# Kernel tuning notes

Measured on AMD Instinct MI355X. Metric: run time of the kernel, lower is better.

## Reference

```python
import jax, jax.numpy as jnp
import numpy as np
import math

D_MODEL = 1024
N_HEAD = 16
HEAD_DIM = D_MODEL // N_HEAD


def setup_inputs() -> dict:
    key = jax.random.key(0)
    ks = jax.random.split(key, 9)
    B, S = 2, 2048
    x = jax.random.normal(ks[0], (B, S, D_MODEL), dtype=jnp.float32)
    # nn.Linear weights are [out, in]; default-ish init scale 0.02, phase projs std=0.005
    w = lambda k, std: jax.random.normal(k, (D_MODEL, D_MODEL), dtype=jnp.float32) * std
    return {
        "x": x,
        "Wq_amp": w(ks[1], 0.02),
        "Wk_amp": w(ks[2], 0.02),
        "Wq_phi": w(ks[3], 0.005),
        "Wk_phi": w(ks[4], 0.005),
        "Wv": w(ks[5], 0.02),
        "Wo": w(ks[6], 0.02),
        "score_log_scale": jnp.zeros((N_HEAD,), dtype=jnp.float32),
    }


def _split_heads(t):
    B, S, _ = t.shape
    return t.reshape(B, S, N_HEAD, HEAD_DIM).transpose(0, 2, 1, 3)  # [B,H,S,hd]


def reference(x, Wq_amp, Wk_amp, Wq_phi, Wk_phi, Wv, Wo, score_log_scale):
    B, S, _ = x.shape
    eps = 1e-6
    # amplitude (softplus) and phase (pi * tanh) projections
    q_amp = _split_heads(jax.nn.softplus(x @ Wq_amp.T))
    k_amp = _split_heads(jax.nn.softplus(x @ Wk_amp.T))
    q_phi = _split_heads(math.pi * jnp.tanh(x @ Wq_phi.T))
    k_phi = _split_heads(math.pi * jnp.tanh(x @ Wk_phi.T))
    # RMS-normalize amplitudes over head_dim
    q_amp = q_amp / jnp.sqrt(jnp.mean(q_amp * q_amp, axis=-1, keepdims=True) + eps)
    k_amp = k_amp / jnp.sqrt(jnp.mean(k_amp * k_amp, axis=-1, keepdims=True) + eps)
    # interference components
    q_cos = q_amp * jnp.cos(q_phi)
    q_sin = q_amp * jnp.sin(q_phi)
    k_cos = k_amp * jnp.cos(k_phi)
    k_sin = k_amp * jnp.sin(k_phi)
    # two-term score matmul, scaled
    scores = (jnp.einsum("bhqd,bhkd->bhqk", q_cos, k_cos)
              + jnp.einsum("bhqd,bhkd->bhqk", q_sin, k_sin)) / math.sqrt(HEAD_DIM)
    scores = scores * jnp.exp(score_log_scale)[None, :, None, None]
    # causal mask + softmax
    mask = jnp.tril(jnp.ones((S, S), dtype=bool))
    scores = jnp.where(mask[None, None], scores, -jnp.inf)
    attn = jax.nn.softmax(scores, axis=-1)
    v = _split_heads(x @ Wv.T)
    out = jnp.einsum("bhqk,bhkd->bhqd", attn, v)
    out = out.transpose(0, 2, 1, 3).reshape(B, S, D_MODEL)
    return out @ Wo.T
```

## Files before the change

### kernel.cpp

```cpp
#include <hip/hip_runtime.h>
#include <hip/hip_bf16.h>
#include <math.h>

#define S_LEN 2048
#define NH 16
#define HD 64
#define DM 1024
#define NTOK 4096
#define NBH 32

typedef __attribute__((ext_vector_type(8))) __bf16 bf16x8;
typedef __attribute__((ext_vector_type(8))) ushort ushort8;
typedef __attribute__((ext_vector_type(4))) ushort ushort4v;
typedef __attribute__((ext_vector_type(4))) float f32x4;
typedef __attribute__((ext_vector_type(16))) float f32x16;
typedef __attribute__((ext_vector_type(4))) uint u32x4;

__device__ __forceinline__ ushort f2b(float x) {
  __hip_bfloat16 h = __float2bfloat16(x);
  return *reinterpret_cast<ushort*>(&h);
}

__device__ __forceinline__ uint pk2(float lo, float hi) {
  return (uint)f2b(lo) | ((uint)f2b(hi) << 16);
}

__device__ __forceinline__ void gload16b(const void* g, void* l) {
  __builtin_amdgcn_global_load_lds((const __attribute__((address_space(1))) void*)g,
                                   (__attribute__((address_space(3))) void*)l, 16, 0, 0);
}

#define MFMA16(a, b, c) __builtin_amdgcn_mfma_f32_16x16x32_bf16((a), (b), (c), 0, 0, 0)
#define MFMA32(a, b, c) __builtin_amdgcn_mfma_f32_32x32x16_bf16((a), (b), (c), 0, 0, 0)

struct CvtArgs {
  const float* src[7];
  ushort* dst[7];
  int n[7];
};

__global__ void cvt_kernel(CvtArgs a) {
  int arr = blockIdx.y;
  long i = ((long)blockIdx.x * blockDim.x + threadIdx.x) * 8;
  if (i >= a.n[arr]) return;
  const float* s = a.src[arr];
  ushort* d = a.dst[arr];
  float4 v0 = *reinterpret_cast<const float4*>(s + i);
  float4 v1 = *reinterpret_cast<const float4*>(s + i + 4);
  ushort8 r;
  r[0] = f2b(v0.x); r[1] = f2b(v0.y); r[2] = f2b(v0.z); r[3] = f2b(v0.w);
  r[4] = f2b(v1.x); r[5] = f2b(v1.y); r[6] = f2b(v1.z); r[7] = f2b(v1.w);
  *reinterpret_cast<ushort8*>(d + i) = r;
}

__global__ __launch_bounds__(256, 2) void qkproj_kernel(
    const ushort* __restrict__ A,
    const ushort* __restrict__ Wqa, const ushort* __restrict__ Wqp,
    const ushort* __restrict__ Wka, const ushort* __restrict__ Wkp,
    const ushort* __restrict__ Wv, const float* __restrict__ sls,
    ushort* __restrict__ qext, ushort* __restrict__ kext, ushort* __restrict__ vT) {
  __shared__ __align__(16) ushort Alds[2][4096];
  __shared__ __align__(16) ushort B0lds[2][4096];
  __shared__ __align__(16) ushort B1lds[2][4096];
  const int u = blockIdx.x;
  int z, bx, by;
  if (u < 512) { z = u >> 8; int v = u & 255; bx = v & 7; by = v >> 3; }
  else         { z = 2;      int v = u - 512; bx = v & 7; by = v >> 3; }
  const int t = threadIdx.x;
  const int lane = t & 63;
  const int wave = t >> 6;
  const int wm = wave >> 1, wn = wave & 1;
  const int l15 = lane & 15, g = lane >> 4;
  const int mbase = by * 128, nbase = bx * 128;
  const int K = DM;
  const int srow = t >> 2, scol = (t & 3) * 8;
  const ushort* Ag = A + (size_t)(mbase + srow) * K + scol;
  const ushort* Wa = (z == 0) ? Wqa : (z == 1) ? Wka : Wv;
  const ushort* Wp = (z == 0) ? Wqp : Wkp;
  const ushort* Wag = Wa + (size_t)(nbase + srow) * K + scol;
  const ushort* Wpg = (z < 2) ? (Wp + (size_t)(nbase + srow) * K + scol) : Wag;

  const int nk = K / 32;
  f32x4 accA[4][4] = {};

  if (z < 2) {
    f32x4 accP[4][4] = {};
    auto stage = [&](int buf, int kt) {
      gload16b(Ag + kt, &Alds[buf][t * 8]);
      gload16b(Ag + kt + (size_t)64 * K, &Alds[buf][t * 8 + 64 * 32]);
      gload16b(Wag + kt, &B0lds[buf][t * 8]);
      gload16b(Wag + kt + (size_t)64 * K, &B0lds[buf][t * 8 + 64 * 32]);
      gload16b(Wpg + kt, &B1lds[buf][t * 8]);
      gload16b(Wpg + kt + (size_t)64 * K, &B1lds[buf][t * 8 + 64 * 32]);
    };
    stage(0, 0);
    for (int kt = 0; kt < nk; ++kt) {
      const int cur = kt & 1;
      if (kt + 1 < nk) {
        stage(cur ^ 1, (kt + 1) * 32);
        asm volatile("s_waitcnt vmcnt(6)" ::: "memory");
      } else {
        asm volatile("s_waitcnt vmcnt(0)" ::: "memory");
      }
      __builtin_amdgcn_s_barrier();
      bf16x8 af[4], ba[4], bp[4];
#pragma unroll
      for (int i = 0; i < 4; i++)
        af[i] = *reinterpret_cast<const bf16x8*>(&Alds[cur][(wm * 64 + i * 16 + l15) * 32 + g * 8]);
#pragma unroll
      for (int j = 0; j < 4; j++) {
        ba[j] = *reinterpret_cast<const bf16x8*>(&B0lds[cur][(wn * 64 + j * 16 + l15) * 32 + g * 8]);
        bp[j] = *reinterpret_cast<const bf16x8*>(&B1lds[cur][(wn * 64 + j * 16 + l15) * 32 + g * 8]);
      }
      __builtin_amdgcn_s_setprio(1);
#pragma unroll
      for (int i = 0; i < 4; i++)
#pragma unroll
        for (int j = 0; j < 4; j++) {
          accA[i][j] = MFMA16(af[i], ba[j], accA[i][j]);
          accP[i][j] = MFMA16(af[i], bp[j], accP[i][j]);
        }
      __builtin_amdgcn_s_setprio(0);
      __builtin_amdgcn_s_barrier();
    }
    const int row0 = mbase + wm * 64;
    const int h = (nbase >> 6) + wn;
    const float scale = (z == 0) ? __expf(sls[h]) * 0.125f : 1.0f;
    ushort* ext = (z == 0) ? qext : kext;
#pragma unroll
    for (int i = 0; i < 4; i++) {
#pragma unroll
      for (int r = 0; r < 4; r++) {
        float sp[4];
        float ss = 0.0f;
#pragma unroll
        for (int j = 0; j < 4; j++) {
          float v = accA[i][j][r];
          sp[j] = fmaxf(v, 0.0f) + __logf(1.0f + __expf(-fabsf(v)));
          ss += sp[j] * sp[j];
        }
        ss += __shfl_xor(ss, 1);
        ss += __shfl_xor(ss, 2);
        ss += __shfl_xor(ss, 4);
        ss += __shfl_xor(ss, 8);
        float rn = rsqrtf(ss * (1.0f / 64.0f) + 1e-6f) * scale;
        const int token = row0 + i * 16 + g * 4 + r;
        const int bb = token >> 11, sidx = token & 2047;
        ushort* base = ext + (((size_t)(bb * NH + h) * S_LEN + sidx) << 7);
#pragma unroll
        for (int j = 0; j < 4; j++) {
          float e = __expf(2.0f * accP[i][j][r]);
          float th = 1.0f - 2.0f * __builtin_amdgcn_rcpf(e + 1.0f);
          float phi = 3.14159265358979f * th;
          float sn = __sinf(phi), cs = __cosf(phi);
          float a = sp[j] * rn;
          int d = j * 16 + l15;
          base[d] = f2b(a * cs);
          base[64 + d] = f2b(a * sn);
        }
      }
    }
  } else {
    auto stage = [&](int buf, int kt) {
      gload16b(Ag + kt, &Alds[buf][t * 8]);
      gload16b(Ag + kt + (size_t)64 * K, &Alds[buf][t * 8 + 64 * 32]);
      gload16b(Wag + kt, &B0lds[buf][t * 8]);
      gload16b(Wag + kt + (size_t)64 * K, &B0lds[buf][t * 8 + 64 * 32]);
    };
    stage(0, 0);
    for (int kt = 0; kt < nk; ++kt) {
      const int cur = kt & 1;
      if (kt + 1 < nk) {
        stage(cur ^ 1, (kt + 1) * 32);
        asm volatile("s_waitcnt vmcnt(4)" ::: "memory");
      } else {
        asm volatile("s_waitcnt vmcnt(0)" ::: "memory");
      }
      __builtin_amdgcn_s_barrier();
      bf16x8 af[4], ba[4];
#pragma unroll
      for (int i = 0; i < 4; i++)
        af[i] = *reinterpret_cast<const bf16x8*>(&Alds[cur][(wm * 64 + i * 16 + l15) * 32 + g * 8]);
#pragma unroll
      for (int j = 0; j < 4; j++)
        ba[j] = *reinterpret_cast<const bf16x8*>(&B0lds[cur][(wn * 64 + j * 16 + l15) * 32 + g * 8]);
      __builtin_amdgcn_s_setprio(1);
#pragma unroll
      for (int i = 0; i < 4; i++)
#pragma unroll
        for (int j = 0; j < 4; j++)
          accA[i][j] = MFMA16(af[i], ba[j], accA[i][j]);
      __builtin_amdgcn_s_setprio(0);
      __builtin_amdgcn_s_barrier();
    }
    const int row0 = mbase + wm * 64, col0 = nbase + wn * 64;
#pragma unroll
    for (int i = 0; i < 4; i++)
#pragma unroll
      for (int j = 0; j < 4; j++) {
        int col = col0 + j * 16 + l15;
        int h = col >> 6, hd = col & 63;
        int t0 = row0 + i * 16 + g * 4;
        int bb = t0 >> 11, s0 = t0 & 2047;
        ushort4v w;
#pragma unroll
        for (int r = 0; r < 4; r++) w[r] = f2b(accA[i][j][r]);
        *reinterpret_cast<ushort4v*>(
            &vT[(((size_t)(bb * NH + h) * HD + hd) << 11) + s0]) = w;
      }
  }
}

__global__ __launch_bounds__(256) void gemm_bt(const ushort* __restrict__ A,
                                               const ushort* __restrict__ W,
                                               float* __restrict__ Cout,
                                               int M, int N, int K) {
  __shared__ __align__(16) ushort Alds[2 * 4096];
  __shared__ __align__(16) ushort Blds[2 * 4096];
  const int t = threadIdx.x;
  const int lane = t & 63;
  const int wave = t >> 6;
  const int wm = wave >> 1, wn = wave & 1;
  const int l15 = lane & 15, g = lane >> 4;
  const int mbase = blockIdx.y * 128, nbase = blockIdx.x * 128;
  const int srow = t >> 2, scol = (t & 3) * 8;
  const ushort* Ag = A + (size_t)(mbase + srow) * K + scol;
  const ushort* Wg = W + (size_t)(nbase + srow) * K + scol;
  auto stage = [&](int buf, int kt) {
    ushort* Al = Alds + buf * 4096 + t * 8;
    ushort* Bl = Blds + buf * 4096 + t * 8;
    gload16b(Ag + kt, Al);
    gload16b(Ag + kt + (size_t)64 * K, Al + 64 * 32);
    gload16b(Wg + kt, Bl);
    gload16b(Wg + kt + (size_t)64 * K, Bl + 64 * 32);
  };
  const int nk = K / 32;
  stage(0, 0);
  f32x4 acc[4][4] = {};
  for (int kt = 0; kt < nk; ++kt) {
    const int cur = kt & 1;
    if (kt + 1 < nk) {
      stage(cur ^ 1, (kt + 1) * 32);
      asm volatile("s_waitcnt vmcnt(4)" ::: "memory");
    } else {
      asm volatile("s_waitcnt vmcnt(0)" ::: "memory");
    }
    __builtin_amdgcn_s_barrier();
    const ushort* Ab = Alds + cur * 4096;
    const ushort* Bb = Blds + cur * 4096;
    bf16x8 af[4], bfr[4];
#pragma unroll
    for (int i = 0; i < 4; i++)
      af[i] = *reinterpret_cast<const bf16x8*>(&Ab[(wm * 64 + i * 16 + l15) * 32 + g * 8]);
#pragma unroll
    for (int j = 0; j < 4; j++)
      bfr[j] = *reinterpret_cast<const bf16x8*>(&Bb[(wn * 64 + j * 16 + l15) * 32 + g * 8]);
    __builtin_amdgcn_s_setprio(1);
#pragma unroll
    for (int i = 0; i < 4; i++)
#pragma unroll
      for (int j = 0; j < 4; j++)
        acc[i][j] = MFMA16(af[i], bfr[j], acc[i][j]);
    __builtin_amdgcn_s_setprio(0);
    __builtin_amdgcn_s_barrier();
  }
  const int row0 = mbase + wm * 64, col0 = nbase + wn * 64;
#pragma unroll
  for (int i = 0; i < 4; i++)
#pragma unroll
    for (int j = 0; j < 4; j++)
#pragma unroll
      for (int r = 0; r < 4; r++) {
        int row = row0 + i * 16 + g * 4 + r;
        int col = col0 + j * 16 + l15;
        Cout[(size_t)row * N + col] = acc[i][j][r];
      }
}

__device__ __forceinline__ void stage_kv(const char* Kp, const char* Vp, int kb,
                                         char* buf, int wave, int lane) {
#pragma unroll
  for (int c = 0; c < 4; c++) {
    int i = wave * 4 + c;
    int kvl = i * 4 + (lane >> 4);
    int slot = (lane & 15) ^ (kvl & 7);
    gload16b(Kp + (size_t)(kb + kvl) * 256 + slot * 16, buf + i * 1024);
  }
#pragma unroll
  for (int c = 0; c < 2; c++) {
    int i = wave * 2 + c;
    int hd = i * 8 + (lane >> 3);
    int slot = (lane & 7) ^ (hd & 7);
    gload16b(Vp + (size_t)hd * (S_LEN * 2) + (size_t)kb * 2 + slot * 16,
             buf + 16384 + i * 1024);
  }
}

__global__ __launch_bounds__(256, 2) void attn_kernel(const ushort* __restrict__ qext,
                                                      const ushort* __restrict__ kext,
                                                      const ushort* __restrict__ vT,
                                                      ushort* __restrict__ attnout) {
  __shared__ __align__(16) char lds[2][24576];
  const int u = blockIdx.x;
  const int uh = u >> 8, v = u & 255;
  const int bh = v >> 3, j = v & 7;
  const int qt = uh ? (15 - j) : j;
  const int b = bh >> 4, h = bh & 15;
  const int wave = threadIdx.x >> 6, lane = threadIdx.x & 63;
  const int l31 = lane & 31, hi = lane >> 5;
  const int qb = qt * 128;
  const int qw = qb + wave * 32;
  const int qa = qw + l31;
  const char* Kp = (const char*)(kext + (size_t)bh * S_LEN * 128);
  const char* Vp = (const char*)(vT + (size_t)bh * HD * S_LEN);
  const ushort* Qp = qext + (size_t)bh * S_LEN * 128;
  const int nt = 2 * qt + 2;
  const int ksw = l31 & 7;

  stage_kv(Kp, Vp, 0, lds[0], wave, lane);
  bf16x8 qf[8];
#pragma unroll
  for (int s = 0; s < 8; s++)
    qf[s] = *reinterpret_cast<const bf16x8*>(&Qp[(size_t)qa * 128 + s * 16 + hi * 8]);

  f32x16 o0 = {}, o1 = {};
  float m = -1e30f, ls = 0.0f;

  for (int t = 0; t < nt; ++t) {
    const int cur = t & 1;
    const int kb = t << 6;
    if (t + 1 < nt) {
      stage_kv(Kp, Vp, (t + 1) << 6, lds[cur ^ 1], wave, lane);
      asm volatile("s_waitcnt vmcnt(6)" ::: "memory");
    } else {
      asm volatile("s_waitcnt vmcnt(0)" ::: "memory");
    }
    __builtin_amdgcn_s_barrier();

    const char* Kb = lds[cur];
    const char* Vb = lds[cur] + 16384;

    f32x16 st0 = {}, st1 = {};
    __builtin_amdgcn_s_setprio(1);
#pragma unroll
    for (int s = 0; s < 8; s++) {
      int sl = ((s * 2 + hi) ^ ksw) << 4;
      bf16x8 k0 = *(const bf16x8*)(Kb + l31 * 256 + sl);
      bf16x8 k1 = *(const bf16x8*)(Kb + (32 + l31) * 256 + sl);
      st0 = MFMA32(k0, qf[s], st0);
      st1 = MFMA32(k1, qf[s], st1);
    }
    __builtin_amdgcn_s_setprio(0);

    if (kb + 64 > qw) {
#pragma unroll
      for (int r = 0; r < 16; r++) {
        int kv = kb + (r & 3) + 8 * (r >> 2) + 4 * hi;
        if (kv > qa) st0[r] = -1e30f;
        if (kv + 32 > qa) st1[r] = -1e30f;
      }
    }
    float pm = -1e30f;
#pragma unroll
    for (int r = 0; r < 16; r++) pm = fmaxf(pm, fmaxf(st0[r], st1[r]));
    pm = fmaxf(pm, __shfl_xor(pm, 32));
    if (!__all(pm <= m + 8.0f)) {
      float mn = fmaxf(m, pm);
      float corr = __expf(m - mn);
      m = mn;
      ls *= corr;
#pragma unroll
      for (int r = 0; r < 16; r++) { o0[r] *= corr; o1[r] *= corr; }
    }
    float ssum = 0.0f;
#pragma unroll
    for (int r = 0; r < 16; r++) {
      st0[r] = __expf(st0[r] - m);
      st1[r] = __expf(st1[r] - m);
      ssum += st0[r] + st1[r];
    }
    ssum += __shfl_xor(ssum, 32);
    ls += ssum;

    u32x4 pb[4];
#pragma unroll
    for (int half = 0; half < 2; half++) {
      const f32x16& st = half ? st1 : st0;
      uint cA0 = pk2(st[0], st[1]),  cA1 = pk2(st[2], st[3]);
      uint cB0 = pk2(st[4], st[5]),  cB1 = pk2(st[6], st[7]);
      uint cC0 = pk2(st[8], st[9]),  cC1 = pk2(st[10], st[11]);
      uint cD0 = pk2(st[12], st[13]), cD1 = pk2(st[14], st[15]);
      uint xA0 = __shfl_xor(cA0, 32), xA1 = __shfl_xor(cA1, 32);
      uint xB0 = __shfl_xor(cB0, 32), xB1 = __shfl_xor(cB1, 32);
      uint xC0 = __shfl_xor(cC0, 32), xC1 = __shfl_xor(cC1, 32);
      uint xD0 = __shfl_xor(cD0, 32), xD1 = __shfl_xor(cD1, 32);
      u32x4 lo, hi4;
      lo[0] = cA0; lo[1] = cA1; lo[2] = xA0; lo[3] = xA1;
      hi4[0] = xB0; hi4[1] = xB1; hi4[2] = cB0; hi4[3] = cB1;
      pb[half * 2] = hi ? hi4 : lo;
      u32x4 lo2, hi2;
      lo2[0] = cC0; lo2[1] = cC1; lo2[2] = xC0; lo2[3] = xC1;
      hi2[0] = xD0; hi2[1] = xD1; hi2[2] = cD0; hi2[3] = cD1;
      pb[half * 2 + 1] = hi ? hi2 : lo2;
    }
    __builtin_amdgcn_s_setprio(1);
#pragma unroll
    for (int ks = 0; ks < 4; ks++) {
      int sl = ((ks * 2 + hi) ^ ksw) << 4;
      bf16x8 v0 = *(const bf16x8*)(Vb + l31 * 128 + sl);
      bf16x8 v1 = *(const bf16x8*)(Vb + (32 + l31) * 128 + sl);
      bf16x8 pbb = *reinterpret_cast<const bf16x8*>(&pb[ks]);
      o0 = MFMA32(v0, pbb, o0);
      o1 = MFMA32(v1, pbb, o1);
    }
    __builtin_amdgcn_s_setprio(0);
    __builtin_amdgcn_s_barrier();
  }

  float inv = 1.0f / ls;
  ushort* Op = attnout + ((size_t)b * S_LEN + qa) * DM + h * HD;
#pragma unroll
  for (int g4 = 0; g4 < 4; g4++) {
    ushort4v w0, w1;
#pragma unroll
    for (int jj = 0; jj < 4; jj++) {
      w0[jj] = f2b(o0[4 * g4 + jj] * inv);
      w1[jj] = f2b(o1[4 * g4 + jj] * inv);
    }
    *reinterpret_cast<ushort4v*>(Op + 8 * g4 + 4 * hi) = w0;
    *reinterpret_cast<ushort4v*>(Op + 32 + 8 * g4 + 4 * hi) = w1;
  }
}

extern "C" void kernel_launch(void* const* d_in, const int* in_sizes, int n_in,
                              void* d_out, int out_size, void* d_ws, size_t ws_size,
                              hipStream_t stream) {
  const float* x   = (const float*)d_in[0];
  const float* Wqa = (const float*)d_in[1];
  const float* Wka = (const float*)d_in[2];
  const float* Wqp = (const float*)d_in[3];
  const float* Wkp = (const float*)d_in[4];
  const float* Wv  = (const float*)d_in[5];
  const float* Wo  = (const float*)d_in[6];
  const float* sls = (const float*)d_in[7];

  char* ws = (char*)d_ws;
  ushort* x_bf = (ushort*)ws; ws += (size_t)NTOK * DM * 2;
  ushort* w_bf[6];
  for (int i = 0; i < 6; i++) { w_bf[i] = (ushort*)ws; ws += (size_t)DM * DM * 2; }
  ushort* qext = (ushort*)ws; ws += (size_t)NBH * S_LEN * 128 * 2;
  ushort* kext = (ushort*)ws; ws += (size_t)NBH * S_LEN * 128 * 2;
  ushort* vT   = (ushort*)ws; ws += (size_t)NBH * HD * S_LEN * 2;
  ushort* attn = (ushort*)ws; ws += (size_t)NTOK * DM * 2;

  CvtArgs ca;
  ca.src[0] = x; ca.dst[0] = x_bf; ca.n[0] = NTOK * DM;
  const float* wsrc[6] = {Wqa, Wka, Wqp, Wkp, Wv, Wo};
  for (int i = 0; i < 6; i++) { ca.src[i + 1] = wsrc[i]; ca.dst[i + 1] = w_bf[i]; ca.n[i + 1] = DM * DM; }
  dim3 cg((NTOK * DM / 8 + 255) / 256, 7);
  hipLaunchKernelGGL(cvt_kernel, cg, dim3(256), 0, stream, ca);

  hipLaunchKernelGGL(qkproj_kernel, dim3(768), dim3(256), 0, stream,
                     x_bf, w_bf[0], w_bf[2], w_bf[1], w_bf[3], w_bf[4], sls,
                     qext, kext, vT);

  hipLaunchKernelGGL(attn_kernel, dim3(512), dim3(256), 0, stream,
                     qext, kext, vT, attn);

  dim3 gg(DM / 128, NTOK / 128);
  hipLaunchKernelGGL(gemm_bt, gg, dim3(256), 0, stream, attn, w_bf[5], (float*)d_out,
                     NTOK, DM, DM);
}
```

Baseline: 164.3 us.

## XOR-swizzle GEMM LDS tiles and remap blocks across XCDs for L2 locality

The projection and output GEMM kernels now store A/B tiles in LDS with an XOR swizzle on the 16-byte column chunk, and read fragments through the matching swizzle. This is meant to cut LDS bank conflicts on the MFMA fragment reads. Both kernels also remap the linear block index so that consecutive blocks dispatched round-robin to the 8 XCDs work on contiguous tiles, which should improve L2 reuse. The output GEMM moves from a 2D grid to a 1D grid to support this remapping. The risk is small, limited to index arithmetic and to getting the swizzle consistent between the LDS stores and loads.

```diff
diff --git a/kernel.cpp b/kernel.cpp
--- a/kernel.cpp
+++ b/kernel.cpp
@@ -62,7 +62,9 @@
   __shared__ __align__(16) ushort Alds[2][4096];
   __shared__ __align__(16) ushort B0lds[2][4096];
   __shared__ __align__(16) ushort B1lds[2][4096];
-  const int u = blockIdx.x;
+  const int d = blockIdx.x;
+  const int xc = d & 7, c = d >> 3;
+  const int u = (c < 64) ? (xc * 64 + c) : (512 + xc * 32 + (c - 64));
   int z, bx, by;
   if (u < 512) { z = u >> 8; int v = u & 255; bx = v & 7; by = v >> 3; }
   else         { z = 2;      int v = u - 512; bx = v & 7; by = v >> 3; }
@@ -73,7 +75,10 @@
   const int l15 = lane & 15, g = lane >> 4;
   const int mbase = by * 128, nbase = bx * 128;
   const int K = DM;
-  const int srow = t >> 2, scol = (t & 3) * 8;
+  const int srow = t >> 2;
+  const int sx = (srow >> 1) & 3;
+  const int scol = (((t & 3) ^ sx)) * 8;
+  const int xr = (l15 >> 1) & 3;
   const ushort* Ag = A + (size_t)(mbase + srow) * K + scol;
   const ushort* Wa = (z == 0) ? Wqa : (z == 1) ? Wka : Wv;
   const ushort* Wp = (z == 0) ? Wqp : Wkp;
@@ -106,11 +111,14 @@
       bf16x8 af[4], ba[4], bp[4];
 #pragma unroll
       for (int i = 0; i < 4; i++)
-        af[i] = *reinterpret_cast<const bf16x8*>(&Alds[cur][(wm * 64 + i * 16 + l15) * 32 + g * 8]);
+        af[i] = *reinterpret_cast<const bf16x8*>(
+            &Alds[cur][(wm * 64 + i * 16 + l15) * 32 + (g ^ xr) * 8]);
 #pragma unroll
       for (int j = 0; j < 4; j++) {
-        ba[j] = *reinterpret_cast<const bf16x8*>(&B0lds[cur][(wn * 64 + j * 16 + l15) * 32 + g * 8]);
-        bp[j] = *reinterpret_cast<const bf16x8*>(&B1lds[cur][(wn * 64 + j * 16 + l15) * 32 + g * 8]);
+        ba[j] = *reinterpret_cast<const bf16x8*>(
+            &B0lds[cur][(wn * 64 + j * 16 + l15) * 32 + (g ^ xr) * 8]);
+        bp[j] = *reinterpret_cast<const bf16x8*>(
+            &B1lds[cur][(wn * 64 + j * 16 + l15) * 32 + (g ^ xr) * 8]);
       }
       __builtin_amdgcn_s_setprio(1);
 #pragma unroll
@@ -154,9 +162,9 @@
           float phi = 3.14159265358979f * th;
           float sn = __sinf(phi), cs = __cosf(phi);
           float a = sp[j] * rn;
-          int d = j * 16 + l15;
-          base[d] = f2b(a * cs);
-          base[64 + d] = f2b(a * sn);
+          int dd = j * 16 + l15;
+          base[dd] = f2b(a * cs);
+          base[64 + dd] = f2b(a * sn);
         }
       }
     }
@@ -180,10 +188,12 @@
       bf16x8 af[4], ba[4];
 #pragma unroll
       for (int i = 0; i < 4; i++)
-        af[i] = *reinterpret_cast<const bf16x8*>(&Alds[cur][(wm * 64 + i * 16 + l15) * 32 + g * 8]);
+        af[i] = *reinterpret_cast<const bf16x8*>(
+            &Alds[cur][(wm * 64 + i * 16 + l15) * 32 + (g ^ xr) * 8]);
 #pragma unroll
       for (int j = 0; j < 4; j++)
-        ba[j] = *reinterpret_cast<const bf16x8*>(&B0lds[cur][(wn * 64 + j * 16 + l15) * 32 + g * 8]);
+        ba[j] = *reinterpret_cast<const bf16x8*>(
+            &B0lds[cur][(wn * 64 + j * 16 + l15) * 32 + (g ^ xr) * 8]);
       __builtin_amdgcn_s_setprio(1);
 #pragma unroll
       for (int i = 0; i < 4; i++)
@@ -217,13 +227,19 @@
                                                int M, int N, int K) {
   __shared__ __align__(16) ushort Alds[2 * 4096];
   __shared__ __align__(16) ushort Blds[2 * 4096];
+  const int d = blockIdx.x;
+  const int u = (d & 7) * 32 + (d >> 3);
+  const int bx = u & 7, by = u >> 3;
   const int t = threadIdx.x;
   const int lane = t & 63;
   const int wave = t >> 6;
   const int wm = wave >> 1, wn = wave & 1;
   const int l15 = lane & 15, g = lane >> 4;
-  const int mbase = blockIdx.y * 128, nbase = blockIdx.x * 128;
-  const int srow = t >> 2, scol = (t & 3) * 8;
+  const int mbase = by * 128, nbase = bx * 128;
+  const int srow = t >> 2;
+  const int sx = (srow >> 1) & 3;
+  const int scol = (((t & 3) ^ sx)) * 8;
+  const int xr = (l15 >> 1) & 3;
   const ushort* Ag = A + (size_t)(mbase + srow) * K + scol;
   const ushort* Wg = W + (size_t)(nbase + srow) * K + scol;
   auto stage = [&](int buf, int kt) {
@@ -251,10 +267,12 @@
     bf16x8 af[4], bfr[4];
 #pragma unroll
     for (int i = 0; i < 4; i++)
-      af[i] = *reinterpret_cast<const bf16x8*>(&Ab[(wm * 64 + i * 16 + l15) * 32 + g * 8]);
+      af[i] = *reinterpret_cast<const bf16x8*>(
+          &Ab[(wm * 64 + i * 16 + l15) * 32 + (g ^ xr) * 8]);
 #pragma unroll
     for (int j = 0; j < 4; j++)
-      bfr[j] = *reinterpret_cast<const bf16x8*>(&Bb[(wn * 64 + j * 16 + l15) * 32 + g * 8]);
+      bfr[j] = *reinterpret_cast<const bf16x8*>(
+          &Bb[(wn * 64 + j * 16 + l15) * 32 + (g ^ xr) * 8]);
     __builtin_amdgcn_s_setprio(1);
 #pragma unroll
     for (int i = 0; i < 4; i++)
@@ -467,7 +485,6 @@
   hipLaunchKernelGGL(attn_kernel, dim3(512), dim3(256), 0, stream,
                      qext, kext, vT, attn);
 
-  dim3 gg(DM / 128, NTOK / 128);
-  hipLaunchKernelGGL(gemm_bt, gg, dim3(256), 0, stream, attn, w_bf[5], (float*)d_out,
-                     NTOK, DM, DM);
-}
+  hipLaunchKernelGGL(gemm_bt, dim3(256), dim3(256), 0, stream, attn, w_bf[5],
+                     (float*)d_out, NTOK, DM, DM);
+}
```

Result: faster. 157.7 us (-4.0%).
